# Optimization experiments

Hardware: AMD Instinct MI355X
Metric: run time of the kernel (lower is better)

The kernel has to match this reference:

```python
import jax, jax.numpy as jnp
import numpy as np

EMBED_DIM = 1024
FFN_DIM = 4096
N_QUBITS = 16
BATCH, SEQ = 4, 2048


def setup_inputs() -> dict:
    key = jax.random.key(0)
    ks = jax.random.split(key, 6)
    s1 = 1.0 / np.sqrt(EMBED_DIM)
    s2 = 1.0 / np.sqrt(FFN_DIM)
    s3 = 1.0 / np.sqrt(N_QUBITS)
    return {
        "x": jax.random.normal(ks[0], (BATCH, SEQ, EMBED_DIM), jnp.float32),
        "W1": jax.random.normal(ks[1], (FFN_DIM, EMBED_DIM), jnp.float32) * s1,
        "Wq": jax.random.normal(ks[2], (N_QUBITS, FFN_DIM), jnp.float32) * s2,
        "theta": jax.random.normal(ks[3], (N_QUBITS,), jnp.float32),
        "W2": jax.random.normal(ks[4], (FFN_DIM, N_QUBITS), jnp.float32) * s3,
        "Wo": jax.random.normal(ks[5], (EMBED_DIM, FFN_DIM), jnp.float32) * s2,
    }


def reference(x, W1, Wq, theta, W2, Wo):
    # linear1: [b,s,e] @ [f,e]^T -> [b,s,f]
    h = jnp.einsum('bse,fe->bsf', x, W1)
    # to_qubits: [b,s,f] -> [b,s,q]
    q = jnp.einsum('bsf,qf->bsq', h, Wq)
    # Quantum circuit: RX(q_i) encoding then trainable RX(theta_i) per wire,
    # wires are unentangled product states -> <Z_i> = cos(q_i + theta_i).
    qm = jnp.cos(q + theta)
    # linear2 + relu
    h2 = jax.nn.relu(jnp.einsum('bsq,fq->bsf', qm, W2))
    # out_proj (dropout is identity in eval / p=0)
    return jnp.einsum('bsf,ef->bse', h2, Wo)
```

## Files before the change

### kernel.cpp

```cpp
#include <hip/hip_runtime.h>
#include <hip/hip_bf16.h>
#include <math.h>

typedef _Float16 f16;
typedef __attribute__((ext_vector_type(8))) _Float16 f16x8;
typedef __attribute__((ext_vector_type(4))) float f32x4;

#define M_TOT 8192
#define E_DIM 1024
#define F_DIM 4096
#define NQ    16

#define BARRIER() asm volatile("s_barrier" ::: "memory")
#define WAITV(n)  asm volatile("s_waitcnt vmcnt(" #n ")" ::: "memory")

__device__ __forceinline__ f16x8 cvt8(float4 a, float4 b) {
    f16x8 o;
    o[0] = (f16)a.x; o[1] = (f16)a.y; o[2] = (f16)a.z; o[3] = (f16)a.w;
    o[4] = (f16)b.x; o[5] = (f16)b.y; o[6] = (f16)b.z; o[7] = (f16)b.w;
    return o;
}

__global__ __launch_bounds__(256) void cast_wo_kernel(
    const float* __restrict__ wo, f16* __restrict__ woh)
{
    size_t i = ((size_t)blockIdx.x * 256 + threadIdx.x) * 8;
    float4 v0 = *reinterpret_cast<const float4*>(wo + i);
    float4 v1 = *reinterpret_cast<const float4*>(wo + i + 4);
    *reinterpret_cast<f16x8*>(woh + i) = cvt8(v0, v1);
}

__global__ __launch_bounds__(256) void w1t_kernel(
    const float* __restrict__ W1, f16* __restrict__ W1t)
{
    __shared__ float ls[64][68];
    const int bf = blockIdx.x & 63;
    const int be = blockIdx.x >> 6;
    const int t  = threadIdx.x;
    const int r  = t >> 4;
    const int c4 = (t & 15) * 4;
    #pragma unroll
    for (int i = 0; i < 4; ++i) {
        int fr = r + i * 16;
        float4 v = *reinterpret_cast<const float4*>(W1 + (size_t)(bf * 64 + fr) * E_DIM + be * 64 + c4);
        ls[fr][c4] = v.x; ls[fr][c4 + 1] = v.y; ls[fr][c4 + 2] = v.z; ls[fr][c4 + 3] = v.w;
    }
    __syncthreads();
    const int er = t >> 2;
    const int fc = (t & 3) * 16;
    f16x8 o0, o1;
    #pragma unroll
    for (int j = 0; j < 8; ++j) { o0[j] = (f16)ls[fc + j][er]; o1[j] = (f16)ls[fc + 8 + j][er]; }
    f16* dst = W1t + (size_t)(be * 64 + er) * F_DIM + bf * 64 + fc;
    *reinterpret_cast<f16x8*>(dst)     = o0;
    *reinterpret_cast<f16x8*>(dst + 8) = o1;
}

__global__ __launch_bounds__(256) void pad2_kernel(
    const float* __restrict__ W2, f16* __restrict__ w2p)
{
    int t = blockIdx.x * 256 + threadIdx.x;
    size_t i = (size_t)t * 8;
    int row = (int)(i >> 5);
    int col = (int)(i & 31);
    f16x8 o;
    if (col < NQ) {
        float4 v0 = *reinterpret_cast<const float4*>(W2 + (size_t)row * NQ + col);
        float4 v1 = *reinterpret_cast<const float4*>(W2 + (size_t)row * NQ + col + 4);
        o = cvt8(v0, v1);
    } else {
        for (int k = 0; k < 8; ++k) o[k] = (f16)0.f;
    }
    *reinterpret_cast<f16x8*>(w2p + i) = o;
}

__global__ __launch_bounds__(256) void tg_kernel(
    const float* __restrict__ Wq, const f16* __restrict__ W1t,
    float* __restrict__ pT)
{
    const int w = threadIdx.x >> 6, lane = threadIdx.x & 63;
    const int fr = lane & 15, fq = lane >> 4;
    const int kc = blockIdx.x & 15;
    const int et = blockIdx.x >> 4;
    const int e0 = et * 128 + w * 32;
    const int kbase = kc * 256;

    f32x4 acc[2] = {};
    #pragma unroll
    for (int s = 0; s < 8; ++s) {
        int k = kbase + s * 32 + fq * 8;
        float4 a0 = *reinterpret_cast<const float4*>(Wq + (size_t)fr * F_DIM + k);
        float4 a1 = *reinterpret_cast<const float4*>(Wq + (size_t)fr * F_DIM + k + 4);
        f16x8 af = cvt8(a0, a1);
        #pragma unroll
        for (int n = 0; n < 2; ++n) {
            f16x8 bf = *reinterpret_cast<const f16x8*>(W1t + (size_t)(e0 + n * 16 + fr) * F_DIM + k);
            acc[n] = __builtin_amdgcn_mfma_f32_16x16x32_f16(af, bf, acc[n], 0, 0, 0);
        }
    }
    #pragma unroll
    for (int n = 0; n < 2; ++n)
        #pragma unroll
        for (int j = 0; j < 4; ++j)
            pT[(size_t)kc * (16 * E_DIM) + (size_t)(fq * 4 + j) * E_DIM + e0 + n * 16 + fr] = acc[n][j];
}

__global__ __launch_bounds__(256) void treduce_kernel(
    const float* __restrict__ pT, f16* __restrict__ Th)
{
    int idx = blockIdx.x * 256 + threadIdx.x;
    float s = 0.f;
    #pragma unroll
    for (int kc = 0; kc < 16; ++kc) s += pT[(size_t)kc * (16 * E_DIM) + idx];
    Th[idx] = (f16)s;
}

__global__ __launch_bounds__(256) void qx_kernel(
    const float* __restrict__ x, const f16* __restrict__ Th,
    float* __restrict__ pq2)
{
    __shared__ __align__(16) f16 ths[16 * 512];
    const int tid = threadIdx.x, w = tid >> 6, lane = tid & 63;
    const int fr = lane & 15, fq = lane >> 4;
    const int kc = blockIdx.x & 1;
    const int m0 = (blockIdx.x >> 1) * 64;

    #pragma unroll
    for (int i = 0; i < 4; ++i) {
        int tau = i * 256 + tid;
        int q   = tau >> 6;
        int kb  = tau & 63;
        f16x8 v = *reinterpret_cast<const f16x8*>(Th + (size_t)q * E_DIM + kc * 512 + kb * 8);
        int boff = (q * 1024 + kb * 16) ^ ((q & 7) << 4);
        *reinterpret_cast<f16x8*>((char*)ths + boff) = v;
    }
    __syncthreads();

    const int row = m0 + w * 16 + fr;
    const float* xa = x + (size_t)row * E_DIM + kc * 512;
    f32x4 acc = {};
    #pragma unroll
    for (int s = 0; s < 16; ++s) {
        int ko = s * 32 + fq * 8;
        float4 a0 = *reinterpret_cast<const float4*>(xa + ko);
        float4 a1 = *reinterpret_cast<const float4*>(xa + ko + 4);
        f16x8 af = cvt8(a0, a1);
        int boff = (fr * 1024 + ko * 2) ^ ((fr & 7) << 4);
        f16x8 bf = *reinterpret_cast<const f16x8*>((char*)ths + boff);
        acc = __builtin_amdgcn_mfma_f32_16x16x32_f16(af, bf, acc, 0, 0, 0);
    }
    #pragma unroll
    for (int j = 0; j < 4; ++j)
        pq2[(size_t)kc * (M_TOT * NQ) + (size_t)(m0 + w * 16 + fq * 4 + j) * NQ + fr] = acc[j];
}

__global__ __launch_bounds__(256) void qfinal_kernel(
    const float* __restrict__ pq2, const float* __restrict__ theta,
    f16* __restrict__ qmp)
{
    int t = blockIdx.x * 256 + threadIdx.x;
    int row = t >> 4, q = t & 15;
    float s = pq2[t] + pq2[(size_t)M_TOT * NQ + t];
    float v = cosf(s + theta[q]);
    qmp[(size_t)row * 32 + q]      = (f16)v;
    qmp[(size_t)row * 32 + 16 + q] = (f16)0.f;
}

__device__ __forceinline__ void gload_lds16(const f16* g, f16* l) {
    __builtin_amdgcn_global_load_lds(
        (const __attribute__((address_space(1))) void*)(g),
        (__attribute__((address_space(3))) void*)(l), 16, 0, 0);
}

template<typename CT, int SPLIT>
__global__ __launch_bounds__(512, 2)
void gemm8p(const f16* __restrict__ A, const f16* __restrict__ B,
            CT* __restrict__ C, f16* __restrict__ Ch,
            int gx, int K, int lda, int ldb, int ldc)
{
    extern __shared__ __align__(16) f16 smem[];
    const int tid  = threadIdx.x;
    const int w    = tid >> 6;
    const int lane = tid & 63;

    const int nwg = gridDim.x;
    const int bid = blockIdx.x;
    const int cpx = nwg >> 3;
    int swz = (bid & 7) * cpx + (bid >> 3);
    int split = 0, r = swz;
    if (SPLIT) { const int per = nwg >> 1; split = swz / per; r = swz % per; }
    const int by = r / gx, bx = r % gx;
    const int m0 = by * 256, n0 = bx * 256;

    const int wr = w >> 2, wc = w & 3;
    const int fr = lane & 15, fq = lane >> 4;

    const f16* Ab = A + (SPLIT ? (size_t)split * K : (size_t)0);
    const f16* Bb = B + (SPLIT ? (size_t)split * K : (size_t)0);

    const int rl   = w * 8 + (lane >> 3);
    const int scol = (((lane & 7) ^ (rl & 7)) * 8);
    const f16* gA = Ab + (size_t)(m0 + rl) * lda + scol;
    const f16* gB = Bb + (size_t)(n0 + rl) * ldb + scol;
    f16* lA = smem + w * 512;
    f16* lB = smem + 16384 + w * 512;

#define SA(b,h,j,kt) gload_lds16(gA + (size_t)((h)*128 + (j)*64) * lda + (kt), lA + (b)*32768 + (h)*8192 + (j)*4096)
#define SB(b,h,j,kt) gload_lds16(gB + (size_t)((h)*128 + (j)*64) * ldb + (kt), lB + (b)*32768 + (h)*8192 + (j)*4096)
#define SAH(b,h,kt) do { SA(b,h,0,kt); SA(b,h,1,kt); } while(0)
#define SBH(b,h,kt) do { SB(b,h,0,kt); SB(b,h,1,kt); } while(0)

    const int xm  = fr & 7;
    const int so0 = ((0 + fq) ^ xm) * 8;
    const int so1 = ((4 + fq) ^ xm) * 8;
    const int aro = (wr * 128 + fr) * 64;
    const int bro = (wc * 64  + fr) * 64;

#define AF(b,m,ks) (*reinterpret_cast<const f16x8*>(smem + (b)*32768 + aro + (m)*1024 + so##ks))
#define BF(b,n,ks) (*reinterpret_cast<const f16x8*>(smem + (b)*32768 + 16384 + bro + (n)*1024 + so##ks))

    f32x4 acc[8][4] = {};
    f16x8 bf[4][2];

#define PHASE(b, p, STAGES, W4) do {                                              \
    f16x8 a00 = AF(b, 2*(p),   0), a01 = AF(b, 2*(p),   1);                       \
    f16x8 a10 = AF(b, 2*(p)+1, 0), a11 = AF(b, 2*(p)+1, 1);                       \
    if ((p) == 0) { _Pragma("unroll")                                             \
        for (int n = 0; n < 4; ++n) { bf[n][0] = BF(b,n,0); bf[n][1] = BF(b,n,1); } } \
    STAGES;                                                                       \
    BARRIER();                                                                    \
    __builtin_amdgcn_s_setprio(1);                                                \
    _Pragma("unroll") for (int n = 0; n < 4; ++n) {                               \
        acc[2*(p)  ][n] = __builtin_amdgcn_mfma_f32_16x16x32_f16(a00, bf[n][0], acc[2*(p)  ][n], 0,0,0); \
        acc[2*(p)+1][n] = __builtin_amdgcn_mfma_f32_16x16x32_f16(a10, bf[n][0], acc[2*(p)+1][n], 0,0,0); } \
    _Pragma("unroll") for (int n = 0; n < 4; ++n) {                               \
        acc[2*(p)  ][n] = __builtin_amdgcn_mfma_f32_16x16x32_f16(a01, bf[n][1], acc[2*(p)  ][n], 0,0,0); \
        acc[2*(p)+1][n] = __builtin_amdgcn_mfma_f32_16x16x32_f16(a11, bf[n][1], acc[2*(p)+1][n], 0,0,0); } \
    __builtin_amdgcn_s_setprio(0);                                                \
    if (W4) WAITV(4);                                                             \
    BARRIER(); } while(0)

    const int NT = K >> 6;
    const int NI = NT >> 1;

    SAH(0,0,0); SAH(0,1,0);
    SBH(0,0,0); SBH(0,1,0);
    SBH(1,0,64); SBH(1,1,64);
    WAITV(0);
    BARRIER();

    for (int i = 0; i < NI; ++i) {
        const int k1 = (2*i+1) << 6;
        int t2 = 2*i+2; if (t2 > NT-1) t2 = NT-1;
        int t3 = 2*i+3; if (t3 > NT-1) t3 = NT-1;
        const int k2 = t2 << 6, k3 = t3 << 6;
        PHASE(0, 0, SAH(1,0,k1),               0);
        PHASE(0, 1, SAH(1,1,k1); SBH(0,0,k2),  0);
        PHASE(0, 2, SBH(0,1,k2),               0);
        PHASE(0, 3, ,                          1);
        PHASE(1, 0, SAH(0,0,k2),               0);
        PHASE(1, 1, SAH(0,1,k2); SBH(1,0,k3),  0);
        PHASE(1, 2, SBH(1,1,k3),               0);
        PHASE(1, 3, ,                          1);
    }
    WAITV(0);

    #pragma unroll
    for (int m = 0; m < 8; ++m) {
        #pragma unroll
        for (int n = 0; n < 4; ++n) {
            #pragma unroll
            for (int j = 0; j < 4; ++j) {
                int row = m0 + wr * 128 + m * 16 + fq * 4 + j;
                int col = n0 + wc * 64  + n * 16 + fr;
                float v = acc[m][n][j];
                if (SPLIT && split) Ch[(size_t)row * ldc + col] = (f16)v;
                else                C [(size_t)row * ldc + col] = (CT)v;
            }
        }
    }
#undef SA
#undef SB
#undef SAH
#undef SBH
#undef AF
#undef BF
#undef PHASE
}

__global__ __launch_bounds__(256)
void gemm_bt_relu(const f16* __restrict__ A, const f16* __restrict__ B,
                  f16* __restrict__ C, int gx, int K, int lda, int ldb, int ldc)
{
    __shared__ __align__(16) f16 As[128 * 32];
    __shared__ __align__(16) f16 Bs[128 * 32];
    const int tid  = threadIdx.x;
    const int wave = tid >> 6;
    const int lane = tid & 63;
    const int nwg = gridDim.x;
    const int bid = blockIdx.x;
    const int cpx = nwg >> 3;
    int swz = (bid & 7) * cpx + (bid >> 3);
    const int by = swz / gx, bx = swz % gx;
    const int m0 = by * 128, n0 = bx * 128;
    const int wr = wave >> 1, wc = wave & 1;

    const int srow = wave * 32 + (lane >> 2);
    const f16* ag = A + (size_t)(m0 + srow) * lda + (lane & 3) * 8;
    const f16* bg = B + (size_t)(n0 + srow) * ldb + (lane & 3) * 8;
    f16* al0 = As + wave * 1024;
    f16* al1 = As + wave * 1024 + 512;
    f16* bl0 = Bs + wave * 1024;
    f16* bl1 = Bs + wave * 1024 + 512;

    f32x4 acc[4][4] = {};
    const int fr = lane & 15, fq = lane >> 4;

    for (int kt = 0; kt < K; kt += 32) {
        gload_lds16(ag,                    al0);
        gload_lds16(ag + (size_t)16 * lda, al1);
        gload_lds16(bg,                    bl0);
        gload_lds16(bg + (size_t)16 * ldb, bl1);
        ag += 32; bg += 32;
        __syncthreads();
        f16x8 af[4], bff[4];
        #pragma unroll
        for (int mi = 0; mi < 4; ++mi)
            af[mi] = *reinterpret_cast<const f16x8*>(As + (wr * 64 + mi * 16 + fr) * 32 + fq * 8);
        #pragma unroll
        for (int ni = 0; ni < 4; ++ni)
            bff[ni] = *reinterpret_cast<const f16x8*>(Bs + (wc * 64 + ni * 16 + fr) * 32 + fq * 8);
        #pragma unroll
        for (int mi = 0; mi < 4; ++mi)
            #pragma unroll
            for (int ni = 0; ni < 4; ++ni)
                acc[mi][ni] = __builtin_amdgcn_mfma_f32_16x16x32_f16(af[mi], bff[ni], acc[mi][ni], 0, 0, 0);
        __syncthreads();
    }

    #pragma unroll
    for (int mi = 0; mi < 4; ++mi)
        #pragma unroll
        for (int ni = 0; ni < 4; ++ni)
            #pragma unroll
            for (int j = 0; j < 4; ++j) {
                int row = m0 + wr * 64 + mi * 16 + fq * 4 + j;
                int col = n0 + wc * 64 + ni * 16 + fr;
                C[(size_t)row * ldc + col] = (f16)fmaxf(acc[mi][ni][j], 0.f);
            }
}

__global__ __launch_bounds__(256) void out_reduce_kernel(
    float* __restrict__ out, const f16* __restrict__ p1)
{
    size_t i = ((size_t)blockIdx.x * 256 + threadIdx.x) * 8;
    f16x8 p = *reinterpret_cast<const f16x8*>(p1 + i);
    float4 v0 = *reinterpret_cast<const float4*>(out + i);
    float4 v1 = *reinterpret_cast<const float4*>(out + i + 4);
    v0.x += (float)p[0]; v0.y += (float)p[1]; v0.z += (float)p[2]; v0.w += (float)p[3];
    v1.x += (float)p[4]; v1.y += (float)p[5]; v1.z += (float)p[6]; v1.w += (float)p[7];
    *reinterpret_cast<float4*>(out + i)     = v0;
    *reinterpret_cast<float4*>(out + i + 4) = v1;
}

extern "C" void kernel_launch(void* const* d_in, const int* in_sizes, int n_in,
                              void* d_out, int out_size, void* d_ws, size_t ws_size,
                              hipStream_t stream) {
    const float* x  = (const float*)d_in[0];
    const float* W1 = (const float*)d_in[1];
    const float* Wq = (const float*)d_in[2];
    const float* th = (const float*)d_in[3];
    const float* W2 = (const float*)d_in[4];
    const float* Wo = (const float*)d_in[5];
    float* out = (float*)d_out;

    char* base = (char*)d_ws;
    float* pT  = (float*)base;
    f16*   Th  = (f16*)(base + (1 << 20));
    float* pq2 = (float*)(base + (1 << 20) + (1 << 16));
    f16*   p1  = (f16*)base;
    f16*   w1t = (f16*)(base + 16777216);
    f16*   woh = w1t + (size_t)E_DIM * F_DIM;
    f16*   w2p = woh + (size_t)E_DIM * F_DIM;
    f16*   qmp = w2p + (size_t)F_DIM * 32;
    f16*   h2  = qmp + (size_t)M_TOT * 32;

    static bool attr_done = false;
    if (!attr_done) {
        hipFuncSetAttribute((const void*)&gemm8p<float, 1>,
                            hipFuncAttributeMaxDynamicSharedMemorySize, 131072);
        attr_done = true;
    }

    w1t_kernel<<<1024, 256, 0, stream>>>(W1, w1t);
    cast_wo_kernel<<<2048, 256, 0, stream>>>(Wo, woh);
    pad2_kernel<<<64, 256, 0, stream>>>(W2, w2p);
    tg_kernel<<<128, 256, 0, stream>>>(Wq, w1t, pT);
    treduce_kernel<<<64, 256, 0, stream>>>(pT, Th);
    qx_kernel<<<256, 256, 0, stream>>>(x, Th, pq2);
    qfinal_kernel<<<512, 256, 0, stream>>>(pq2, th, qmp);
    gemm_bt_relu<<<2048, 256, 0, stream>>>(qmp, w2p, h2, 32, 32, 32, 32, F_DIM);
    gemm8p<float, 1><<<256, 512, 131072, stream>>>(h2, woh, out, p1, 4, 2048, F_DIM, F_DIM, E_DIM);
    out_reduce_kernel<<<4096, 256, 0, stream>>>(out, p1);
}
```

Measured before the change: 127.0 us.

## Fuse ReLU linear2 producer into out_proj GEMM, dropping h2 intermediate

The separate qm·W2ᵀ+ReLU GEMM no longer writes a full 8192×4096 fp16 h2 activation to global memory. Instead, each out_proj workgroup loads its 256-row qm tile into LDS and builds each 64-wide h2 K-slab on the fly with small MFMAs into the A buffer, interleaved with the B-tile pipeline. This removes one kernel launch and the large h2 write and read, at the cost of recomputing h2 slabs once per column tile, more LDS (144 KiB), extra register use and MFMA work in the main loop. Both split-K halves now write fp16 partials, and the final reduce sums them into the output without first reading it.

```diff
diff --git a/kernel.cpp b/kernel.cpp
--- a/kernel.cpp
+++ b/kernel.cpp
@@ -4,6 +4,7 @@
 
 typedef _Float16 f16;
 typedef __attribute__((ext_vector_type(8))) _Float16 f16x8;
+typedef __attribute__((ext_vector_type(4))) _Float16 f16x4;
 typedef __attribute__((ext_vector_type(4))) float f32x4;
 
 #define M_TOT 8192
@@ -13,6 +14,7 @@
 
 #define BARRIER() asm volatile("s_barrier" ::: "memory")
 #define WAITV(n)  asm volatile("s_waitcnt vmcnt(" #n ")" ::: "memory")
+#define WAITLGKM() asm volatile("s_waitcnt lgkmcnt(0)" ::: "memory")
 
 __device__ __forceinline__ f16x8 cvt8(float4 a, float4 b) {
     f16x8 o;
@@ -172,11 +174,9 @@
         (__attribute__((address_space(3))) void*)(l), 16, 0, 0);
 }
 
-template<typename CT, int SPLIT>
 __global__ __launch_bounds__(512, 2)
-void gemm8p(const f16* __restrict__ A, const f16* __restrict__ B,
-            CT* __restrict__ C, f16* __restrict__ Ch,
-            int gx, int K, int lda, int ldb, int ldc)
+void gemm4f(const f16* __restrict__ qmp, const f16* __restrict__ w2p,
+            const f16* __restrict__ Wo, f16* __restrict__ P0, f16* __restrict__ P1)
 {
     extern __shared__ __align__(16) f16 smem[];
     const int tid  = threadIdx.x;
@@ -187,28 +187,58 @@
     const int bid = blockIdx.x;
     const int cpx = nwg >> 3;
     int swz = (bid & 7) * cpx + (bid >> 3);
-    int split = 0, r = swz;
-    if (SPLIT) { const int per = nwg >> 1; split = swz / per; r = swz % per; }
-    const int by = r / gx, bx = r % gx;
+    const int per = nwg >> 1;
+    const int split = swz / per;
+    const int r = swz % per;
+    const int by = r >> 2, bx = r & 3;
     const int m0 = by * 256, n0 = bx * 256;
 
     const int wr = w >> 2, wc = w & 3;
     const int fr = lane & 15, fq = lane >> 4;
-
-    const f16* Ab = A + (SPLIT ? (size_t)split * K : (size_t)0);
-    const f16* Bb = B + (SPLIT ? (size_t)split * K : (size_t)0);
+    const int K = 2048;
+
+    const f16* Bb  = Wo + (size_t)split * K;
+    const f16* w2g = w2p + (size_t)split * K * 32;
+    f16* Pout = split ? P1 : P0;
 
     const int rl   = w * 8 + (lane >> 3);
     const int scol = (((lane & 7) ^ (rl & 7)) * 8);
-    const f16* gA = Ab + (size_t)(m0 + rl) * lda + scol;
-    const f16* gB = Bb + (size_t)(n0 + rl) * ldb + scol;
-    f16* lA = smem + w * 512;
+    const f16* gB = Bb + (size_t)(n0 + rl) * F_DIM + scol;
     f16* lB = smem + 16384 + w * 512;
 
-#define SA(b,h,j,kt) gload_lds16(gA + (size_t)((h)*128 + (j)*64) * lda + (kt), lA + (b)*32768 + (h)*8192 + (j)*4096)
-#define SB(b,h,j,kt) gload_lds16(gB + (size_t)((h)*128 + (j)*64) * ldb + (kt), lB + (b)*32768 + (h)*8192 + (j)*4096)
-#define SAH(b,h,kt) do { SA(b,h,0,kt); SA(b,h,1,kt); } while(0)
+#define SB(b,h,j,kt) gload_lds16(gB + (size_t)((h)*128 + (j)*64) * F_DIM + (kt), lB + (b)*32768 + (h)*8192 + (j)*4096)
 #define SBH(b,h,kt) do { SB(b,h,0,kt); SB(b,h,1,kt); } while(0)
+
+    f16* qmS = smem + 65536;
+    {
+        const int qrow = w * 16 + (lane >> 2);
+        const f16* qsrc = qmp + (size_t)(m0 + qrow) * 32 + (((lane & 3) ^ (qrow & 3)) << 3);
+        f16* qdst = qmS + w * 512;
+        gload_lds16(qsrc, qdst);
+        gload_lds16(qsrc + 128 * 32, qdst + 4096);
+    }
+
+    f16x8 w2a[4], w2b[4];
+#define LOADW2(R, kt) do { _Pragma("unroll") \
+    for (int ft = 0; ft < 4; ++ft) \
+        R[ft] = *reinterpret_cast<const f16x8*>(w2g + (size_t)((kt) + ft*16 + fr) * 32 + fq * 8); } while(0)
+
+    const int mt0 = 2 * w;
+#define PRODUCE(bdst, W2R) do {                                                   \
+    const int r0_ = mt0 * 16 + fr, r1_ = r0_ + 16;                                \
+    f16x8 q0_ = *reinterpret_cast<const f16x8*>(qmS + r0_ * 32 + ((fq ^ (fr & 3)) << 3)); \
+    f16x8 q1_ = *reinterpret_cast<const f16x8*>(qmS + r1_ * 32 + ((fq ^ (fr & 3)) << 3)); \
+    f32x4 z_ = {0.f, 0.f, 0.f, 0.f};                                              \
+    _Pragma("unroll") for (int ft = 0; ft < 4; ++ft) {                            \
+        f32x4 c0_ = __builtin_amdgcn_mfma_f32_16x16x32_f16(W2R[ft], q0_, z_, 0, 0, 0); \
+        f32x4 c1_ = __builtin_amdgcn_mfma_f32_16x16x32_f16(W2R[ft], q1_, z_, 0, 0, 0); \
+        f16x4 h0_, h1_;                                                           \
+        _Pragma("unroll") for (int jj = 0; jj < 4; ++jj) {                        \
+            h0_[jj] = (f16)fmaxf(c0_[jj], 0.f); h1_[jj] = (f16)fmaxf(c1_[jj], 0.f); } \
+        const int sl_ = (2 * ft + (fq >> 1)) ^ (fr & 7);                          \
+        *reinterpret_cast<f16x4*>(smem + (bdst)*32768 + r0_*64 + sl_*8 + ((fq & 1) << 2)) = h0_; \
+        *reinterpret_cast<f16x4*>(smem + (bdst)*32768 + r1_*64 + sl_*8 + ((fq & 1) << 2)) = h1_; \
+    } } while(0)
 
     const int xm  = fr & 7;
     const int so0 = ((0 + fq) ^ xm) * 8;
@@ -237,16 +267,20 @@
         acc[2*(p)  ][n] = __builtin_amdgcn_mfma_f32_16x16x32_f16(a01, bf[n][1], acc[2*(p)  ][n], 0,0,0); \
         acc[2*(p)+1][n] = __builtin_amdgcn_mfma_f32_16x16x32_f16(a11, bf[n][1], acc[2*(p)+1][n], 0,0,0); } \
     __builtin_amdgcn_s_setprio(0);                                                \
-    if (W4) WAITV(4);                                                             \
+    if (W4) { WAITV(8); WAITLGKM(); }                                             \
     BARRIER(); } while(0)
 
     const int NT = K >> 6;
     const int NI = NT >> 1;
 
-    SAH(0,0,0); SAH(0,1,0);
-    SBH(0,0,0); SBH(0,1,0);
+    LOADW2(w2b, 0);
+    LOADW2(w2a, 64);
+    SBH(0,0,0);  SBH(0,1,0);
     SBH(1,0,64); SBH(1,1,64);
     WAITV(0);
+    BARRIER();
+    PRODUCE(0, w2b);
+    WAITLGKM();
     BARRIER();
 
     for (int i = 0; i < NI; ++i) {
@@ -254,14 +288,14 @@
         int t2 = 2*i+2; if (t2 > NT-1) t2 = NT-1;
         int t3 = 2*i+3; if (t3 > NT-1) t3 = NT-1;
         const int k2 = t2 << 6, k3 = t3 << 6;
-        PHASE(0, 0, SAH(1,0,k1),               0);
-        PHASE(0, 1, SAH(1,1,k1); SBH(0,0,k2),  0);
-        PHASE(0, 2, SBH(0,1,k2),               0);
-        PHASE(0, 3, ,                          1);
-        PHASE(1, 0, SAH(0,0,k2),               0);
-        PHASE(1, 1, SAH(0,1,k2); SBH(1,0,k3),  0);
-        PHASE(1, 2, SBH(1,1,k3),               0);
-        PHASE(1, 3, ,                          1);
+        PHASE(0, 0, PRODUCE(1, w2a),            0);
+        PHASE(0, 1, LOADW2(w2b, k2); SBH(0,0,k2), 0);
+        PHASE(0, 2, SBH(0,1,k2),                0);
+        PHASE(0, 3, ,                           1);
+        PHASE(1, 0, PRODUCE(0, w2b),            0);
+        PHASE(1, 1, LOADW2(w2a, k3); SBH(1,0,k3), 0);
+        PHASE(1, 2, SBH(1,1,k3),                0);
+        PHASE(1, 3, ,                           1);
     }
     WAITV(0);
 
@@ -273,92 +307,30 @@
             for (int j = 0; j < 4; ++j) {
                 int row = m0 + wr * 128 + m * 16 + fq * 4 + j;
                 int col = n0 + wc * 64  + n * 16 + fr;
-                float v = acc[m][n][j];
-                if (SPLIT && split) Ch[(size_t)row * ldc + col] = (f16)v;
-                else                C [(size_t)row * ldc + col] = (CT)v;
+                Pout[(size_t)row * E_DIM + col] = (f16)acc[m][n][j];
             }
         }
     }
-#undef SA
 #undef SB
-#undef SAH
 #undef SBH
+#undef LOADW2
+#undef PRODUCE
 #undef AF
 #undef BF
 #undef PHASE
 }
 
-__global__ __launch_bounds__(256)
-void gemm_bt_relu(const f16* __restrict__ A, const f16* __restrict__ B,
-                  f16* __restrict__ C, int gx, int K, int lda, int ldb, int ldc)
-{
-    __shared__ __align__(16) f16 As[128 * 32];
-    __shared__ __align__(16) f16 Bs[128 * 32];
-    const int tid  = threadIdx.x;
-    const int wave = tid >> 6;
-    const int lane = tid & 63;
-    const int nwg = gridDim.x;
-    const int bid = blockIdx.x;
-    const int cpx = nwg >> 3;
-    int swz = (bid & 7) * cpx + (bid >> 3);
-    const int by = swz / gx, bx = swz % gx;
-    const int m0 = by * 128, n0 = bx * 128;
-    const int wr = wave >> 1, wc = wave & 1;
-
-    const int srow = wave * 32 + (lane >> 2);
-    const f16* ag = A + (size_t)(m0 + srow) * lda + (lane & 3) * 8;
-    const f16* bg = B + (size_t)(n0 + srow) * ldb + (lane & 3) * 8;
-    f16* al0 = As + wave * 1024;
-    f16* al1 = As + wave * 1024 + 512;
-    f16* bl0 = Bs + wave * 1024;
-    f16* bl1 = Bs + wave * 1024 + 512;
-
-    f32x4 acc[4][4] = {};
-    const int fr = lane & 15, fq = lane >> 4;
-
-    for (int kt = 0; kt < K; kt += 32) {
-        gload_lds16(ag,                    al0);
-        gload_lds16(ag + (size_t)16 * lda, al1);
-        gload_lds16(bg,                    bl0);
-        gload_lds16(bg + (size_t)16 * ldb, bl1);
-        ag += 32; bg += 32;
-        __syncthreads();
-        f16x8 af[4], bff[4];
-        #pragma unroll
-        for (int mi = 0; mi < 4; ++mi)
-            af[mi] = *reinterpret_cast<const f16x8*>(As + (wr * 64 + mi * 16 + fr) * 32 + fq * 8);
-        #pragma unroll
-        for (int ni = 0; ni < 4; ++ni)
-            bff[ni] = *reinterpret_cast<const f16x8*>(Bs + (wc * 64 + ni * 16 + fr) * 32 + fq * 8);
-        #pragma unroll
-        for (int mi = 0; mi < 4; ++mi)
-            #pragma unroll
-            for (int ni = 0; ni < 4; ++ni)
-                acc[mi][ni] = __builtin_amdgcn_mfma_f32_16x16x32_f16(af[mi], bff[ni], acc[mi][ni], 0, 0, 0);
-        __syncthreads();
-    }
-
-    #pragma unroll
-    for (int mi = 0; mi < 4; ++mi)
-        #pragma unroll
-        for (int ni = 0; ni < 4; ++ni)
-            #pragma unroll
-            for (int j = 0; j < 4; ++j) {
-                int row = m0 + wr * 64 + mi * 16 + fq * 4 + j;
-                int col = n0 + wc * 64 + ni * 16 + fr;
-                C[(size_t)row * ldc + col] = (f16)fmaxf(acc[mi][ni][j], 0.f);
-            }
-}
-
-__global__ __launch_bounds__(256) void out_reduce_kernel(
-    float* __restrict__ out, const f16* __restrict__ p1)
+__global__ __launch_bounds__(256) void out_reduce2_kernel(
+    float* __restrict__ out, const f16* __restrict__ p0, const f16* __restrict__ p1)
 {
     size_t i = ((size_t)blockIdx.x * 256 + threadIdx.x) * 8;
-    f16x8 p = *reinterpret_cast<const f16x8*>(p1 + i);
-    float4 v0 = *reinterpret_cast<const float4*>(out + i);
-    float4 v1 = *reinterpret_cast<const float4*>(out + i + 4);
-    v0.x += (float)p[0]; v0.y += (float)p[1]; v0.z += (float)p[2]; v0.w += (float)p[3];
-    v1.x += (float)p[4]; v1.y += (float)p[5]; v1.z += (float)p[6]; v1.w += (float)p[7];
+    f16x8 a = *reinterpret_cast<const f16x8*>(p0 + i);
+    f16x8 b = *reinterpret_cast<const f16x8*>(p1 + i);
+    float4 v0, v1;
+    v0.x = (float)a[0] + (float)b[0]; v0.y = (float)a[1] + (float)b[1];
+    v0.z = (float)a[2] + (float)b[2]; v0.w = (float)a[3] + (float)b[3];
+    v1.x = (float)a[4] + (float)b[4]; v1.y = (float)a[5] + (float)b[5];
+    v1.z = (float)a[6] + (float)b[6]; v1.w = (float)a[7] + (float)b[7];
     *reinterpret_cast<float4*>(out + i)     = v0;
     *reinterpret_cast<float4*>(out + i + 4) = v1;
 }
@@ -378,17 +350,17 @@
     float* pT  = (float*)base;
     f16*   Th  = (f16*)(base + (1 << 20));
     float* pq2 = (float*)(base + (1 << 20) + (1 << 16));
-    f16*   p1  = (f16*)base;
     f16*   w1t = (f16*)(base + 16777216);
     f16*   woh = w1t + (size_t)E_DIM * F_DIM;
     f16*   w2p = woh + (size_t)E_DIM * F_DIM;
     f16*   qmp = w2p + (size_t)F_DIM * 32;
-    f16*   h2  = qmp + (size_t)M_TOT * 32;
+    f16*   p0  = qmp + (size_t)M_TOT * 32;
+    f16*   p1  = p0  + (size_t)M_TOT * E_DIM;
 
     static bool attr_done = false;
     if (!attr_done) {
-        hipFuncSetAttribute((const void*)&gemm8p<float, 1>,
-                            hipFuncAttributeMaxDynamicSharedMemorySize, 131072);
+        hipFuncSetAttribute((const void*)&gemm4f,
+                            hipFuncAttributeMaxDynamicSharedMemorySize, 147456);
         attr_done = true;
     }
 
@@ -399,7 +371,6 @@
     treduce_kernel<<<64, 256, 0, stream>>>(pT, Th);
     qx_kernel<<<256, 256, 0, stream>>>(x, Th, pq2);
     qfinal_kernel<<<512, 256, 0, stream>>>(pq2, th, qmp);
-    gemm_bt_relu<<<2048, 256, 0, stream>>>(qmp, w2p, h2, 32, 32, 32, 32, F_DIM);
-    gemm8p<float, 1><<<256, 512, 131072, stream>>>(h2, woh, out, p1, 4, 2048, F_DIM, F_DIM, E_DIM);
-    out_reduce_kernel<<<4096, 256, 0, stream>>>(out, p1);
-}
+    gemm4f<<<256, 512, 147456, stream>>>(qmp, w2p, woh, p0, p1);
+    out_reduce2_kernel<<<4096, 256, 0, stream>>>(out, p0, p1);
+}
```

Measured after the change: 122.2 us. 1.04x faster.
